# Optimization experiments

Hardware: AMD Instinct MI355X
Metric: run time of the kernel (lower is better)

Reference implementation:

```python
import jax, jax.numpy as jnp
import numpy as np


def _bitlinear(x, w_latent):
    # per-output-row abs-mean scale, ternary round with straight-through estimator
    scale = jax.lax.stop_gradient(
        jnp.clip(jnp.mean(jnp.abs(w_latent), axis=1, keepdims=True), 1e-5, None))
    tern = jnp.clip(jnp.round(w_latent / scale), -1.0, 1.0)
    w = w_latent + jax.lax.stop_gradient(tern - w_latent)  # STE
    return x @ (w * scale).T


def setup_inputs() -> dict:
    key = jax.random.key(0)
    ks = jax.random.split(key, 6)
    dim, hidden, rank = 1024, 4096, 16
    B, S = 4, 4096
    x = jax.random.normal(ks[0], (B, S, dim), dtype=jnp.float32)
    w_fc = 0.02 * jax.random.normal(ks[1], (hidden, dim), dtype=jnp.float32)
    w_proj = 0.02 * jax.random.normal(ks[2], (dim, hidden), dtype=jnp.float32)
    u = 0.02 * jax.random.normal(ks[3], (hidden, rank), dtype=jnp.float32)
    v = 0.02 * jax.random.normal(ks[4], (rank, dim), dtype=jnp.float32)
    fast_b = jax.random.normal(ks[5], (rank, rank), dtype=jnp.float32)
    gate = jnp.float32(0.05)
    return {"x": x, "fast_b": fast_b, "w_fc": w_fc, "w_proj": w_proj,
            "u": u, "v": v, "gate": gate}


def reference(x, fast_b, w_fc, w_proj, u, v, gate):
    # fc BitLinear + low-rank fast adapter delta
    h = _bitlinear(x, w_fc) + gate * (((x @ v.T) @ fast_b.T) @ u.T)
    r = jnp.maximum(h, 0.0)
    return _bitlinear(r * r, w_proj)  # ReLU^2 then proj BitLinear
```

## Files before the change

### kernel.cpp

```cpp
#include <hip/hip_runtime.h>


typedef unsigned short u16;
typedef __attribute__((ext_vector_type(8))) short short8;
typedef __attribute__((ext_vector_type(4))) float float4v;

#define M_TOK   16384
#define DIM     1024
#define HID     4096


__device__ __forceinline__ u16 f2bf(float f) {
    union { float f; unsigned u; } v; v.f = f;
    unsigned r = v.u + 0x7fffu + ((v.u >> 16) & 1u);
    return (u16)(r >> 16);
}

__device__ __forceinline__ void gload_lds16(const u16* g, u16* l) {
    __builtin_amdgcn_global_load_lds(
        (const __attribute__((address_space(1))) void*)g,
        (__attribute__((address_space(3))) void*)l, 16, 0, 0);
}


__global__ __launch_bounds__(256) void prologue_kernel(
    const float* __restrict__ x, const float* __restrict__ w_fc,
    const float* __restrict__ w_proj, const float* __restrict__ u,
    const float* __restrict__ fb, const float* __restrict__ v,
    const float* __restrict__ gate,
    u16* __restrict__ Xb, u16* __restrict__ W1, u16* __restrict__ W2) {
    const int b = blockIdx.x, tid = threadIdx.x;
    __shared__ float red[4];

    if (b < HID) {
        const int row = b;
        float s = 0.f;
#pragma unroll
        for (int jj = 0; jj < 4; jj++) s += fabsf(w_fc[row * 1024 + tid + jj * 256]);
#pragma unroll
        for (int o = 32; o > 0; o >>= 1) s += __shfl_down(s, o, 64);
        if ((tid & 63) == 0) red[tid >> 6] = s;
        __syncthreads();
        const float scale = fmaxf((red[0] + red[1] + red[2] + red[3]) * (1.f / 1024.f), 1e-5f);
        const float g = gate[0];
        float t[16];
#pragma unroll
        for (int r = 0; r < 16; r++) t[r] = 0.f;
#pragma unroll
        for (int k = 0; k < 16; k++) {
            const float uk = u[row * 16 + k];
#pragma unroll
            for (int r = 0; r < 16; r++) t[r] += uk * fb[k * 16 + r];
        }
#pragma unroll
        for (int jj = 0; jj < 4; jj++) {
            const int j = tid + jj * 256;
            const float wv = w_fc[row * 1024 + j];
            float tern = rintf(wv / scale);
            tern = fminf(1.f, fmaxf(-1.f, tern));
            float ad = 0.f;
#pragma unroll
            for (int r = 0; r < 16; r++) ad += t[r] * v[r * 1024 + j];
            W1[row * 1024 + j] = f2bf(tern * scale + g * ad);
        }
    } else if (b < HID + DIM) {
        const int row = b - HID;
        float s = 0.f;
#pragma unroll
        for (int jj = 0; jj < 16; jj++) s += fabsf(w_proj[row * 4096 + tid + jj * 256]);
#pragma unroll
        for (int o = 32; o > 0; o >>= 1) s += __shfl_down(s, o, 64);
        if ((tid & 63) == 0) red[tid >> 6] = s;
        __syncthreads();
        const float scale = fmaxf((red[0] + red[1] + red[2] + red[3]) * (1.f / 4096.f), 1e-5f);
#pragma unroll
        for (int jj = 0; jj < 16; jj++) {
            const int j = tid + jj * 256;
            float tern = rintf(w_proj[row * 4096 + j] / scale);
            tern = fminf(1.f, fmaxf(-1.f, tern));
            W2[row * 4096 + j] = f2bf(tern * scale);
        }
    } else {
        const int i = (b - (HID + DIM)) * 1024 + tid * 4;
        float4 vv = *reinterpret_cast<const float4*>(x + i);
        ushort4 o;
        o.x = f2bf(vv.x); o.y = f2bf(vv.y); o.z = f2bf(vv.z); o.w = f2bf(vv.w);
        *reinterpret_cast<ushort4*>(Xb + i) = o;
    }
}

template <int N, int K, int EPI>
__global__ __launch_bounds__(512, 2) void gemm256(const u16* __restrict__ A,
                                                  const u16* __restrict__ B,
                                                  void* __restrict__ Cv) {
    constexpr int GM  = M_TOK / 256;
    constexpr int GN  = N / 256;
    constexpr int NWG = GM * GN;
    constexpr int NT  = K / 64;

    __shared__ alignas(16) u16 lds[2][2][256 * 64];

    const int tid  = threadIdx.x;
    const int wave = tid >> 6, lane = tid & 63;
    const int lr = lane & 15, quad = lane >> 4;
    const int wm = (wave >> 2) << 7;
    const int wn = (wave & 3) << 6;

    int flat = (int)blockIdx.x;
    flat = (flat & 7) * (NWG / 8) + (flat >> 3);
    const int bm = flat % GM;
    const int bn = flat / GM;

    const u16* Ag[4]; const u16* Bg[4]; int qo[4];
#pragma unroll
    for (int c = 0; c < 4; c++) {
        const int q = tid + c * 512;
        const int row = q >> 3, p = q & 7;
        const int kc = p ^ (row & 7);
        Ag[c] = A + (size_t)(bm * 256 + row) * K + kc * 8;
        Bg[c] = B + (size_t)(bn * 256 + row) * K + kc * 8;
        qo[c] = q * 8;
    }

    float4v acc[8][4];
#pragma unroll
    for (int i = 0; i < 8; i++)
#pragma unroll
        for (int j = 0; j < 4; j++) acc[i][j] = (float4v)0.0f;

    const int pk0 = (quad ^ (lr & 7)) * 8;
    const int pk1 = ((4 + quad) ^ (lr & 7)) * 8;
    const int aoff = (wm + lr) * 64;
    const int boff = (wn + lr) * 64;

#define STAGE(buf, k0)                                                        \
    do {                                                                      \
        u16* la_ = &lds[buf][0][0]; u16* lb_ = &lds[buf][1][0];               \
        _Pragma("unroll")                                                     \
        for (int c_ = 0; c_ < 4; c_++) gload_lds16(Ag[c_] + (k0), la_ + qo[c_]); \
        _Pragma("unroll")                                                     \
        for (int c_ = 0; c_ < 4; c_++) gload_lds16(Bg[c_] + (k0), lb_ + qo[c_]); \
    } while (0)

#define SB() __builtin_amdgcn_sched_barrier(0)

#define CLUSTER8(ri, cj, Af, Bf)                                              \
    do {                                                                      \
        SB();                                                                 \
        __builtin_amdgcn_s_setprio(1);                                        \
        _Pragma("unroll")                                                     \
        for (int i_ = 0; i_ < 4; i_++) {                                      \
            acc[(ri) + i_][(cj) + 0] = __builtin_amdgcn_mfma_f32_16x16x32_bf16( \
                Af[i_], Bf[0], acc[(ri) + i_][(cj) + 0], 0, 0, 0);            \
            acc[(ri) + i_][(cj) + 1] = __builtin_amdgcn_mfma_f32_16x16x32_bf16( \
                Af[i_], Bf[1], acc[(ri) + i_][(cj) + 1], 0, 0, 0);            \
        }                                                                     \
        __builtin_amdgcn_s_setprio(0);                                        \
        SB();                                                                 \
    } while (0)

    short8 A0[4], A1[4], B0v[2], B1v[2];
    short8 C0[4], C1[4], D0v[2], D1v[2];

    STAGE(0, 0);
    STAGE(1, 64);
    SB();
    asm volatile("s_waitcnt vmcnt(8)" ::: "memory");
    __builtin_amdgcn_s_barrier();
    SB();
    {
        const u16* Ab = &lds[0][0][0]; const u16* Bb = &lds[0][1][0];
#pragma unroll
        for (int i = 0; i < 4; i++) A0[i]  = *reinterpret_cast<const short8*>(Ab + aoff + 1024 * i + pk0);
#pragma unroll
        for (int j = 0; j < 2; j++) B0v[j] = *reinterpret_cast<const short8*>(Bb + boff + 1024 * j + pk0);
    }

    for (int t = 0; t < NT; ++t) {
        const int cur = t & 1, nxt = cur ^ 1;
        const u16* Ab = &lds[cur][0][0];
        const u16* Bb = &lds[cur][1][0];

#pragma unroll
        for (int j = 0; j < 2; j++) B1v[j] = *reinterpret_cast<const short8*>(Bb + boff + 2048 + 1024 * j + pk0);
        CLUSTER8(0, 0, A0, B0v);

#pragma unroll
        for (int i = 0; i < 4; i++) A1[i] = *reinterpret_cast<const short8*>(Ab + aoff + 4096 + 1024 * i + pk0);
        CLUSTER8(0, 2, A0, B1v);

#pragma unroll
        for (int i = 0; i < 4; i++) C0[i] = *reinterpret_cast<const short8*>(Ab + aoff + 1024 * i + pk1);
        CLUSTER8(4, 0, A1, B0v);

#pragma unroll
        for (int j = 0; j < 2; j++) D0v[j] = *reinterpret_cast<const short8*>(Bb + boff + 1024 * j + pk1);
        CLUSTER8(4, 2, A1, B1v);

#pragma unroll
        for (int j = 0; j < 2; j++) D1v[j] = *reinterpret_cast<const short8*>(Bb + boff + 2048 + 1024 * j + pk1);
        CLUSTER8(0, 0, C0, D0v);

#pragma unroll
        for (int i = 0; i < 4; i++) C1[i] = *reinterpret_cast<const short8*>(Ab + aoff + 4096 + 1024 * i + pk1);
        CLUSTER8(0, 2, C0, D1v);

        CLUSTER8(4, 0, C1, D0v);

        SB();
        __builtin_amdgcn_s_barrier();
        SB();
        if (t + 2 < NT) STAGE(cur, (t + 2) * 64);
        SB();
        if (t + 1 < NT) {
            if (t + 2 < NT) {
                asm volatile("s_waitcnt vmcnt(8)" ::: "memory");
            } else {
                asm volatile("s_waitcnt vmcnt(0)" ::: "memory");
            }
            SB();
            __builtin_amdgcn_s_barrier();
            SB();
            const u16* An = &lds[nxt][0][0]; const u16* Bn = &lds[nxt][1][0];
#pragma unroll
            for (int i = 0; i < 4; i++) A0[i]  = *reinterpret_cast<const short8*>(An + aoff + 1024 * i + pk0);
#pragma unroll
            for (int j = 0; j < 2; j++) B0v[j] = *reinterpret_cast<const short8*>(Bn + boff + 1024 * j + pk0);
        }

        CLUSTER8(4, 2, C1, D1v);
    }
#undef STAGE
#undef SB
#undef CLUSTER8

    const int row0 = bm * 256 + wm + quad * 4;
    const int col0 = bn * 256 + wn + lr;
#pragma unroll
    for (int qr = 0; qr < 2; qr++)
#pragma unroll
        for (int i = 0; i < 4; i++)
#pragma unroll
            for (int qc = 0; qc < 2; qc++)
#pragma unroll
                for (int j = 0; j < 2; j++) {
                    const int col = col0 + qc * 32 + j * 16;
                    const float4v a = acc[qr * 4 + i][qc * 2 + j];
#pragma unroll
                    for (int r = 0; r < 4; r++) {
                        const int row = row0 + qr * 64 + i * 16 + r;
                        if (EPI == 0) {
                            const float rr = fmaxf(a[r], 0.f);
                            ((u16*)Cv)[(size_t)row * N + col] = f2bf(rr * rr);
                        } else {
                            ((float*)Cv)[(size_t)row * N + col] = a[r];
                        }
                    }
                }
}


extern "C" void kernel_launch(void* const* d_in, const int* in_sizes, int n_in,
                              void* d_out, int out_size, void* d_ws, size_t ws_size,
                              hipStream_t stream) {
    const float* x      = (const float*)d_in[0];
    const float* fast_b = (const float*)d_in[1];
    const float* w_fc   = (const float*)d_in[2];
    const float* w_proj = (const float*)d_in[3];
    const float* u      = (const float*)d_in[4];
    const float* v      = (const float*)d_in[5];
    const float* gate   = (const float*)d_in[6];
    float* out = (float*)d_out;

    char* ws = (char*)d_ws;
    u16*   Xb  = (u16*)(ws + 0);
    u16*   W1  = (u16*)(ws + 33554432);
    u16*   W2  = (u16*)(ws + 41943040);
    u16*   RSQ = (u16*)(ws + 50331648);

    prologue_kernel<<<HID + DIM + M_TOK * DIM / (256 * 4), 256, 0, stream>>>(
        x, w_fc, w_proj, u, fast_b, v, gate, Xb, W1, W2);

    gemm256<HID, DIM, 0><<<dim3((M_TOK / 256) * (HID / 256)), 512, 0, stream>>>(Xb, W1, RSQ);
    gemm256<DIM, HID, 1><<<dim3((M_TOK / 256) * (DIM / 256)), 512, 0, stream>>>(RSQ, W2, out);
}
```

Measured before the change: 395.2 us.

## Restructure GEMM main loop into 8-phase ping-pong schedule with per-half staging

Replaces the cluster-based double-buffered K loop with a loop unrolled by two K tiles. Each tile is split into four MFMA phases, and each phase is separated by workgroup barriers and explicit lgkm/vm waitcnts. Global-to-LDS loads are issued in half-tile pieces, one per phase, so memory traffic is spread across the compute. The aim is a finer, HipKittens-style interleave of loads and MFMA across waves, at the cost of many more s_barrier calls per iteration and a dependence on NT being even.

```diff
diff --git a/kernel.cpp b/kernel.cpp
--- a/kernel.cpp
+++ b/kernel.cpp
@@ -133,106 +133,137 @@
     const int aoff = (wm + lr) * 64;
     const int boff = (wn + lr) * 64;
 
-#define STAGE(buf, k0)                                                        \
+#define CFENCE() asm volatile("" ::: "memory")
+#define BARX()  do { CFENCE(); __builtin_amdgcn_s_barrier(); CFENCE(); } while (0)
+#define WLG0()  asm volatile("s_waitcnt lgkmcnt(0)" ::: "memory")
+#define WLG8()  asm volatile("s_waitcnt lgkmcnt(8)" ::: "memory")
+#define WVM4()  asm volatile("s_waitcnt vmcnt(4)" ::: "memory")
+#define WVM0()  asm volatile("s_waitcnt vmcnt(0)" ::: "memory")
+
+#define STAGE_HALF(buf, mat, h, k0)                                           \
     do {                                                                      \
-        u16* la_ = &lds[buf][0][0]; u16* lb_ = &lds[buf][1][0];               \
-        _Pragma("unroll")                                                     \
-        for (int c_ = 0; c_ < 4; c_++) gload_lds16(Ag[c_] + (k0), la_ + qo[c_]); \
-        _Pragma("unroll")                                                     \
-        for (int c_ = 0; c_ < 4; c_++) gload_lds16(Bg[c_] + (k0), lb_ + qo[c_]); \
+        u16* lp_ = &lds[buf][mat][0];                                         \
+        gload_lds16(((mat) == 0 ? Ag[2*(h)]   : Bg[2*(h)])   + (k0),          \
+                    lp_ + qo[2*(h)]);                                         \
+        gload_lds16(((mat) == 0 ? Ag[2*(h)+1] : Bg[2*(h)+1]) + (k0),          \
+                    lp_ + qo[2*(h)+1]);                                       \
     } while (0)
 
-#define SB() __builtin_amdgcn_sched_barrier(0)
-
-#define CLUSTER8(ri, cj, Af, Bf)                                              \
+#define READ_A(dst, Ab, hioff)                                                \
+    _Pragma("unroll")                                                         \
+    for (int i_ = 0; i_ < 4; i_++) {                                          \
+        dst[i_][0] = *reinterpret_cast<const short8*>((Ab) + aoff + (hioff) + 1024 * i_ + pk0); \
+        dst[i_][1] = *reinterpret_cast<const short8*>((Ab) + aoff + (hioff) + 1024 * i_ + pk1); \
+    }
+#define READ_B(dst, Bb, hioff)                                                \
+    _Pragma("unroll")                                                         \
+    for (int j_ = 0; j_ < 2; j_++) {                                          \
+        dst[j_][0] = *reinterpret_cast<const short8*>((Bb) + boff + (hioff) + 1024 * j_ + pk0); \
+        dst[j_][1] = *reinterpret_cast<const short8*>((Bb) + boff + (hioff) + 1024 * j_ + pk1); \
+    }
+
+#define MFMA16(qr, qc, Af, Bf)                                                \
     do {                                                                      \
-        SB();                                                                 \
         __builtin_amdgcn_s_setprio(1);                                        \
         _Pragma("unroll")                                                     \
-        for (int i_ = 0; i_ < 4; i_++) {                                      \
-            acc[(ri) + i_][(cj) + 0] = __builtin_amdgcn_mfma_f32_16x16x32_bf16( \
-                Af[i_], Bf[0], acc[(ri) + i_][(cj) + 0], 0, 0, 0);            \
-            acc[(ri) + i_][(cj) + 1] = __builtin_amdgcn_mfma_f32_16x16x32_bf16( \
-                Af[i_], Bf[1], acc[(ri) + i_][(cj) + 1], 0, 0, 0);            \
-        }                                                                     \
+        for (int ks_ = 0; ks_ < 2; ks_++)                                     \
+            _Pragma("unroll")                                                 \
+            for (int i_ = 0; i_ < 4; i_++)                                    \
+                _Pragma("unroll")                                             \
+                for (int j_ = 0; j_ < 2; j_++)                                \
+                    acc[(qr) * 4 + i_][(qc) * 2 + j_] =                       \
+                        __builtin_amdgcn_mfma_f32_16x16x32_bf16(              \
+                            Af[i_][ks_], Bf[j_][ks_],                         \
+                            acc[(qr) * 4 + i_][(qc) * 2 + j_], 0, 0, 0);      \
         __builtin_amdgcn_s_setprio(0);                                        \
-        SB();                                                                 \
     } while (0)
 
-    short8 A0[4], A1[4], B0v[2], B1v[2];
-    short8 C0[4], C1[4], D0v[2], D1v[2];
-
-    STAGE(0, 0);
-    STAGE(1, 64);
-    SB();
-    asm volatile("s_waitcnt vmcnt(8)" ::: "memory");
-    __builtin_amdgcn_s_barrier();
-    SB();
-    {
-        const u16* Ab = &lds[0][0][0]; const u16* Bb = &lds[0][1][0];
-#pragma unroll
-        for (int i = 0; i < 4; i++) A0[i]  = *reinterpret_cast<const short8*>(Ab + aoff + 1024 * i + pk0);
-#pragma unroll
-        for (int j = 0; j < 2; j++) B0v[j] = *reinterpret_cast<const short8*>(Bb + boff + 1024 * j + pk0);
-    }
-
-    for (int t = 0; t < NT; ++t) {
-        const int cur = t & 1, nxt = cur ^ 1;
-        const u16* Ab = &lds[cur][0][0];
-        const u16* Bb = &lds[cur][1][0];
-
-#pragma unroll
-        for (int j = 0; j < 2; j++) B1v[j] = *reinterpret_cast<const short8*>(Bb + boff + 2048 + 1024 * j + pk0);
-        CLUSTER8(0, 0, A0, B0v);
-
-#pragma unroll
-        for (int i = 0; i < 4; i++) A1[i] = *reinterpret_cast<const short8*>(Ab + aoff + 4096 + 1024 * i + pk0);
-        CLUSTER8(0, 2, A0, B1v);
-
-#pragma unroll
-        for (int i = 0; i < 4; i++) C0[i] = *reinterpret_cast<const short8*>(Ab + aoff + 1024 * i + pk1);
-        CLUSTER8(4, 0, A1, B0v);
-
-#pragma unroll
-        for (int j = 0; j < 2; j++) D0v[j] = *reinterpret_cast<const short8*>(Bb + boff + 1024 * j + pk1);
-        CLUSTER8(4, 2, A1, B1v);
-
-#pragma unroll
-        for (int j = 0; j < 2; j++) D1v[j] = *reinterpret_cast<const short8*>(Bb + boff + 2048 + 1024 * j + pk1);
-        CLUSTER8(0, 0, C0, D0v);
-
-#pragma unroll
-        for (int i = 0; i < 4; i++) C1[i] = *reinterpret_cast<const short8*>(Ab + aoff + 4096 + 1024 * i + pk1);
-        CLUSTER8(0, 2, C0, D1v);
-
-        CLUSTER8(4, 0, C1, D0v);
-
-        SB();
-        __builtin_amdgcn_s_barrier();
-        SB();
-        if (t + 2 < NT) STAGE(cur, (t + 2) * 64);
-        SB();
-        if (t + 1 < NT) {
-            if (t + 2 < NT) {
-                asm volatile("s_waitcnt vmcnt(8)" ::: "memory");
-            } else {
-                asm volatile("s_waitcnt vmcnt(0)" ::: "memory");
-            }
-            SB();
-            __builtin_amdgcn_s_barrier();
-            SB();
-            const u16* An = &lds[nxt][0][0]; const u16* Bn = &lds[nxt][1][0];
-#pragma unroll
-            for (int i = 0; i < 4; i++) A0[i]  = *reinterpret_cast<const short8*>(An + aoff + 1024 * i + pk0);
-#pragma unroll
-            for (int j = 0; j < 2; j++) B0v[j] = *reinterpret_cast<const short8*>(Bn + boff + 1024 * j + pk0);
-        }
-
-        CLUSTER8(4, 2, C1, D1v);
-    }
-#undef STAGE
-#undef SB
-#undef CLUSTER8
+    short8 Alo[4][2], Ahi[4][2], Blo[2][2], Bhi[2][2];
+
+    STAGE_HALF(0, 0, 0, 0);  STAGE_HALF(0, 0, 1, 0);
+    STAGE_HALF(0, 1, 0, 0);  STAGE_HALF(0, 1, 1, 0);
+    STAGE_HALF(1, 1, 0, 64); STAGE_HALF(1, 1, 1, 64);
+    WVM4();
+    BARX();
+
+    const u16* A0b = &lds[0][0][0]; const u16* B0b = &lds[0][1][0];
+    const u16* A1b = &lds[1][0][0]; const u16* B1b = &lds[1][1][0];
+
+    for (int it = 0; it < NT / 2; ++it) {
+        const int t0 = 2 * it;
+
+        READ_A(Alo, A0b, 0);
+        READ_B(Blo, B0b, 0);
+        STAGE_HALF(1, 0, 0, (t0 + 1) * 64);
+        WLG8();
+        BARX(); WLG0();
+        MFMA16(0, 0, Alo, Blo);
+        BARX();
+
+        READ_B(Bhi, B0b, 2048);
+        STAGE_HALF(1, 0, 1, (t0 + 1) * 64);
+        BARX(); WLG0();
+        MFMA16(0, 1, Alo, Bhi);
+        BARX();
+
+        READ_A(Ahi, A0b, 4096);
+        if (t0 + 2 < NT) STAGE_HALF(0, 1, 0, (t0 + 2) * 64);
+        BARX(); WLG0();
+        MFMA16(1, 0, Ahi, Blo);
+        BARX();
+
+        if (t0 + 2 < NT) {
+            STAGE_HALF(0, 1, 1, (t0 + 2) * 64);
+            WVM4();
+        } else {
+            WVM0();
+        }
+        BARX();
+        MFMA16(1, 1, Ahi, Bhi);
+        BARX();
+
+        READ_A(Alo, A1b, 0);
+        READ_B(Blo, B1b, 0);
+        if (t0 + 2 < NT) STAGE_HALF(0, 0, 0, (t0 + 2) * 64);
+        WLG8();
+        BARX(); WLG0();
+        MFMA16(0, 0, Alo, Blo);
+        BARX();
+
+        READ_B(Bhi, B1b, 2048);
+        if (t0 + 2 < NT) STAGE_HALF(0, 0, 1, (t0 + 2) * 64);
+        BARX(); WLG0();
+        MFMA16(0, 1, Alo, Bhi);
+        BARX();
+
+        READ_A(Ahi, A1b, 4096);
+        if (t0 + 3 < NT) STAGE_HALF(1, 1, 0, (t0 + 3) * 64);
+        BARX(); WLG0();
+        MFMA16(1, 0, Ahi, Blo);
+        BARX();
+
+        if (t0 + 3 < NT) {
+            STAGE_HALF(1, 1, 1, (t0 + 3) * 64);
+            WVM4();
+        } else {
+            WVM0();
+        }
+        BARX();
+        MFMA16(1, 1, Ahi, Bhi);
+        BARX();
+    }
+    WVM0();
+
+#undef CFENCE
+#undef BARX
+#undef WLG0
+#undef WLG8
+#undef WVM4
+#undef WVM0
+#undef STAGE_HALF
+#undef READ_A
+#undef READ_B
+#undef MFMA16
 
     const int row0 = bm * 256 + wm + quad * 4;
     const int col0 = bn * 256 + wn + lr;
```

Result: no change. 395.2 us (-0.0%).

## Switch GEMM to 4-wave 256x256 tiles with 128x128 per-wave subtiles

Applied to the files above, without the earlier changes.

Replaces the 8-wave block (each wave computing 128x64) with a 4-wave block where each wave computes a 128x128 subtile, doubling accumulators per wave. It also drops the hand-interleaved LDS-load/MFMA clusters and priority hints in favour of loading all fragments, then running a plain MFMA loop per k-step. The intent is more register-level reuse per LDS read, at the cost of fewer waves per block and one block per CU. The simpler schedule gives up the explicit overlap of LDS reads with MFMAs and may raise register pressure.

```diff
diff --git a/kernel.cpp b/kernel.cpp
--- a/kernel.cpp
+++ b/kernel.cpp
@@ -90,7 +90,7 @@
 }
 
 template <int N, int K, int EPI>
-__global__ __launch_bounds__(512, 2) void gemm256(const u16* __restrict__ A,
+__global__ __launch_bounds__(256, 1) void gemm_w4(const u16* __restrict__ A,
                                                   const u16* __restrict__ B,
                                                   void* __restrict__ Cv) {
     constexpr int GM  = M_TOK / 256;
@@ -103,160 +103,117 @@
     const int tid  = threadIdx.x;
     const int wave = tid >> 6, lane = tid & 63;
     const int lr = lane & 15, quad = lane >> 4;
-    const int wm = (wave >> 2) << 7;
-    const int wn = (wave & 3) << 6;
+    const int wm = (wave >> 1) << 7;
+    const int wn = (wave & 1) << 7;
 
     int flat = (int)blockIdx.x;
     flat = (flat & 7) * (NWG / 8) + (flat >> 3);
     const int bm = flat % GM;
     const int bn = flat / GM;
 
-    const u16* Ag[4]; const u16* Bg[4]; int qo[4];
-#pragma unroll
-    for (int c = 0; c < 4; c++) {
-        const int q = tid + c * 512;
-        const int row = q >> 3, p = q & 7;
-        const int kc = p ^ (row & 7);
-        Ag[c] = A + (size_t)(bm * 256 + row) * K + kc * 8;
-        Bg[c] = B + (size_t)(bn * 256 + row) * K + kc * 8;
-        qo[c] = q * 8;
-    }
-
-    float4v acc[8][4];
+    const int r0 = tid >> 3;
+    const int kc = (tid & 7) ^ (r0 & 7);
+    const u16* Ag0 = A + (size_t)(bm * 256 + r0) * K + kc * 8;
+    const u16* Bg0 = B + (size_t)(bn * 256 + r0) * K + kc * 8;
+
+    float4v acc[8][8];
 #pragma unroll
     for (int i = 0; i < 8; i++)
 #pragma unroll
-        for (int j = 0; j < 4; j++) acc[i][j] = (float4v)0.0f;
+        for (int j = 0; j < 8; j++) acc[i][j] = (float4v)0.0f;
 
     const int pk0 = (quad ^ (lr & 7)) * 8;
     const int pk1 = ((4 + quad) ^ (lr & 7)) * 8;
     const int aoff = (wm + lr) * 64;
     const int boff = (wn + lr) * 64;
 
+#define CFENCE() asm volatile("" ::: "memory")
+#define BARX()   do { CFENCE(); __builtin_amdgcn_s_barrier(); CFENCE(); } while (0)
+#define WVM16()  asm volatile("s_waitcnt vmcnt(16)" ::: "memory")
+#define WVM0()   asm volatile("s_waitcnt vmcnt(0)" ::: "memory")
+
 #define STAGE(buf, k0)                                                        \
     do {                                                                      \
-        u16* la_ = &lds[buf][0][0]; u16* lb_ = &lds[buf][1][0];               \
         _Pragma("unroll")                                                     \
-        for (int c_ = 0; c_ < 4; c_++) gload_lds16(Ag[c_] + (k0), la_ + qo[c_]); \
+        for (int c_ = 0; c_ < 8; c_++)                                        \
+            gload_lds16(Ag0 + (size_t)c_ * 32 * K + (k0),                     \
+                        &lds[buf][0][0] + tid * 8 + c_ * 2048);               \
         _Pragma("unroll")                                                     \
-        for (int c_ = 0; c_ < 4; c_++) gload_lds16(Bg[c_] + (k0), lb_ + qo[c_]); \
+        for (int c_ = 0; c_ < 8; c_++)                                        \
+            gload_lds16(Bg0 + (size_t)c_ * 32 * K + (k0),                     \
+                        &lds[buf][1][0] + tid * 8 + c_ * 2048);               \
     } while (0)
-
-#define SB() __builtin_amdgcn_sched_barrier(0)
-
-#define CLUSTER8(ri, cj, Af, Bf)                                              \
-    do {                                                                      \
-        SB();                                                                 \
-        __builtin_amdgcn_s_setprio(1);                                        \
-        _Pragma("unroll")                                                     \
-        for (int i_ = 0; i_ < 4; i_++) {                                      \
-            acc[(ri) + i_][(cj) + 0] = __builtin_amdgcn_mfma_f32_16x16x32_bf16( \
-                Af[i_], Bf[0], acc[(ri) + i_][(cj) + 0], 0, 0, 0);            \
-            acc[(ri) + i_][(cj) + 1] = __builtin_amdgcn_mfma_f32_16x16x32_bf16( \
-                Af[i_], Bf[1], acc[(ri) + i_][(cj) + 1], 0, 0, 0);            \
-        }                                                                     \
-        __builtin_amdgcn_s_setprio(0);                                        \
-        SB();                                                                 \
-    } while (0)
-
-    short8 A0[4], A1[4], B0v[2], B1v[2];
-    short8 C0[4], C1[4], D0v[2], D1v[2];
 
     STAGE(0, 0);
     STAGE(1, 64);
-    SB();
-    asm volatile("s_waitcnt vmcnt(8)" ::: "memory");
-    __builtin_amdgcn_s_barrier();
-    SB();
-    {
-        const u16* Ab = &lds[0][0][0]; const u16* Bb = &lds[0][1][0];
-#pragma unroll
-        for (int i = 0; i < 4; i++) A0[i]  = *reinterpret_cast<const short8*>(Ab + aoff + 1024 * i + pk0);
-#pragma unroll
-        for (int j = 0; j < 2; j++) B0v[j] = *reinterpret_cast<const short8*>(Bb + boff + 1024 * j + pk0);
-    }
-
+    WVM16();
+    BARX();
+
+#pragma unroll 1
     for (int t = 0; t < NT; ++t) {
-        const int cur = t & 1, nxt = cur ^ 1;
+        const int cur = t & 1;
         const u16* Ab = &lds[cur][0][0];
         const u16* Bb = &lds[cur][1][0];
 
-#pragma unroll
-        for (int j = 0; j < 2; j++) B1v[j] = *reinterpret_cast<const short8*>(Bb + boff + 2048 + 1024 * j + pk0);
-        CLUSTER8(0, 0, A0, B0v);
-
-#pragma unroll
-        for (int i = 0; i < 4; i++) A1[i] = *reinterpret_cast<const short8*>(Ab + aoff + 4096 + 1024 * i + pk0);
-        CLUSTER8(0, 2, A0, B1v);
-
-#pragma unroll
-        for (int i = 0; i < 4; i++) C0[i] = *reinterpret_cast<const short8*>(Ab + aoff + 1024 * i + pk1);
-        CLUSTER8(4, 0, A1, B0v);
-
-#pragma unroll
-        for (int j = 0; j < 2; j++) D0v[j] = *reinterpret_cast<const short8*>(Bb + boff + 1024 * j + pk1);
-        CLUSTER8(4, 2, A1, B1v);
-
-#pragma unroll
-        for (int j = 0; j < 2; j++) D1v[j] = *reinterpret_cast<const short8*>(Bb + boff + 2048 + 1024 * j + pk1);
-        CLUSTER8(0, 0, C0, D0v);
-
-#pragma unroll
-        for (int i = 0; i < 4; i++) C1[i] = *reinterpret_cast<const short8*>(Ab + aoff + 4096 + 1024 * i + pk1);
-        CLUSTER8(0, 2, C0, D1v);
-
-        CLUSTER8(4, 0, C1, D0v);
-
-        SB();
-        __builtin_amdgcn_s_barrier();
-        SB();
-        if (t + 2 < NT) STAGE(cur, (t + 2) * 64);
-        SB();
+        short8 Af[8][2], Bf[8][2];
+#pragma unroll
+        for (int i = 0; i < 8; i++) {
+            Af[i][0] = *reinterpret_cast<const short8*>(Ab + aoff + 1024 * i + pk0);
+            Af[i][1] = *reinterpret_cast<const short8*>(Ab + aoff + 1024 * i + pk1);
+        }
+#pragma unroll
+        for (int j = 0; j < 8; j++) {
+            Bf[j][0] = *reinterpret_cast<const short8*>(Bb + boff + 1024 * j + pk0);
+            Bf[j][1] = *reinterpret_cast<const short8*>(Bb + boff + 1024 * j + pk1);
+        }
+
+#pragma unroll
+        for (int ks = 0; ks < 2; ks++)
+#pragma unroll
+            for (int i = 0; i < 8; i++)
+#pragma unroll
+                for (int j = 0; j < 8; j++)
+                    acc[i][j] = __builtin_amdgcn_mfma_f32_16x16x32_bf16(
+                        Af[i][ks], Bf[j][ks], acc[i][j], 0, 0, 0);
+
         if (t + 1 < NT) {
+            BARX();
             if (t + 2 < NT) {
-                asm volatile("s_waitcnt vmcnt(8)" ::: "memory");
+                STAGE(cur, (t + 2) * 64);
+                WVM16();
             } else {
-                asm volatile("s_waitcnt vmcnt(0)" ::: "memory");
+                WVM0();
             }
-            SB();
-            __builtin_amdgcn_s_barrier();
-            SB();
-            const u16* An = &lds[nxt][0][0]; const u16* Bn = &lds[nxt][1][0];
-#pragma unroll
-            for (int i = 0; i < 4; i++) A0[i]  = *reinterpret_cast<const short8*>(An + aoff + 1024 * i + pk0);
-#pragma unroll
-            for (int j = 0; j < 2; j++) B0v[j] = *reinterpret_cast<const short8*>(Bn + boff + 1024 * j + pk0);
-        }
-
-        CLUSTER8(4, 2, C1, D1v);
+            BARX();
+        }
     }
+    WVM0();
+
+#undef CFENCE
+#undef BARX
+#undef WVM16
+#undef WVM0
 #undef STAGE
-#undef SB
-#undef CLUSTER8
 
     const int row0 = bm * 256 + wm + quad * 4;
     const int col0 = bn * 256 + wn + lr;
 #pragma unroll
-    for (int qr = 0; qr < 2; qr++)
-#pragma unroll
-        for (int i = 0; i < 4; i++)
-#pragma unroll
-            for (int qc = 0; qc < 2; qc++)
-#pragma unroll
-                for (int j = 0; j < 2; j++) {
-                    const int col = col0 + qc * 32 + j * 16;
-                    const float4v a = acc[qr * 4 + i][qc * 2 + j];
-#pragma unroll
-                    for (int r = 0; r < 4; r++) {
-                        const int row = row0 + qr * 64 + i * 16 + r;
-                        if (EPI == 0) {
-                            const float rr = fmaxf(a[r], 0.f);
-                            ((u16*)Cv)[(size_t)row * N + col] = f2bf(rr * rr);
-                        } else {
-                            ((float*)Cv)[(size_t)row * N + col] = a[r];
-                        }
-                    }
+    for (int i = 0; i < 8; i++)
+#pragma unroll
+        for (int j = 0; j < 8; j++) {
+            const int col = col0 + j * 16;
+            const float4v a = acc[i][j];
+#pragma unroll
+            for (int r = 0; r < 4; r++) {
+                const int row = row0 + i * 16 + r;
+                if (EPI == 0) {
+                    const float rr = fmaxf(a[r], 0.f);
+                    ((u16*)Cv)[(size_t)row * N + col] = f2bf(rr * rr);
+                } else {
+                    ((float*)Cv)[(size_t)row * N + col] = a[r];
                 }
+            }
+        }
 }
 
 
@@ -281,6 +238,6 @@
     prologue_kernel<<<HID + DIM + M_TOK * DIM / (256 * 4), 256, 0, stream>>>(
         x, w_fc, w_proj, u, fast_b, v, gate, Xb, W1, W2);
 
-    gemm256<HID, DIM, 0><<<dim3((M_TOK / 256) * (HID / 256)), 512, 0, stream>>>(Xb, W1, RSQ);
-    gemm256<DIM, HID, 1><<<dim3((M_TOK / 256) * (DIM / 256)), 512, 0, stream>>>(RSQ, W2, out);
-}
+    gemm_w4<HID, DIM, 0><<<dim3((M_TOK / 256) * (HID / 256)), 256, 0, stream>>>(Xb, W1, RSQ);
+    gemm_w4<DIM, HID, 1><<<dim3((M_TOK / 256) * (DIM / 256)), 256, 0, stream>>>(RSQ, W2, out);
+}
```

After: 533.0 us. +34.9%, slower.
